# Performance work log

Measured on AMD Instinct MI355X. Metric: run time of the kernel, lower is better.

## Reference

```python
import jax, jax.numpy as jnp
import numpy as np

INPUT, HIDDEN, OUTPUT = 256, 512, 256
BATCH, SEQ = 64, 2048


def setup_inputs() -> dict:
    key = jax.random.key(0)
    ks = jax.random.split(key, 5)
    x = jax.random.normal(ks[0], (BATCH, SEQ, INPUT), dtype=jnp.float32)
    W_x = jax.random.normal(ks[1], (INPUT, 4 * HIDDEN), dtype=jnp.float32) * 0.1
    W_h = jax.random.normal(ks[2], (HIDDEN, 4 * HIDDEN), dtype=jnp.float32) * 0.1
    b = jnp.zeros((4 * HIDDEN,), dtype=jnp.float32)
    # fc: nn.Linear(hidden, output) -> weight [OUTPUT, HIDDEN], bias [OUTPUT]
    lim = 1.0 / np.sqrt(HIDDEN)
    fc_w = jax.random.uniform(ks[3], (OUTPUT, HIDDEN), dtype=jnp.float32, minval=-lim, maxval=lim)
    fc_b = jax.random.uniform(ks[4], (OUTPUT,), dtype=jnp.float32, minval=-lim, maxval=lim)
    return {"x": x, "W_x": W_x, "W_h": W_h, "b": b, "fc_w": fc_w, "fc_b": fc_b}


def reference(x, W_x, W_h, b, fc_w, fc_b):
    B, T, _ = x.shape
    H = W_h.shape[0]
    # precompute input projections for all timesteps: [B,T,4H]
    xg = jnp.einsum('bti,ig->btg', x, W_x) + b

    def step(carry, xg_t):
        h, c = carry
        gates = xg_t + h @ W_h  # [B,4H]
        i_t, f_t, g_t, o_t = jnp.split(gates, 4, axis=-1)
        i_t = jax.nn.sigmoid(i_t)
        f_t = jax.nn.sigmoid(f_t)
        g_t = jnp.tanh(g_t)
        o_t = jax.nn.sigmoid(o_t)
        c_new = f_t * c + i_t * g_t
        h_new = o_t * jnp.tanh(c_new)
        return (h_new, c_new), None

    h0 = jnp.zeros((B, H), dtype=x.dtype)
    c0 = jnp.zeros((B, H), dtype=x.dtype)
    (h_t, c_t), _ = jax.lax.scan(step, (h0, c0), jnp.swapaxes(xg, 0, 1))
    y = h_t @ fc_w.T + fc_b
    return y, (h_t, c_t)
```

## Files before the change

### kernel.cpp

```cpp
#include <hip/hip_runtime.h>

#define B_ 64
#define T_ 2048
#define I_ 256
#define H_ 512
#define O_ 256
#define GBC 2
#define GHC 32
#define MB (B_/GBC)
#define HS (H_/GHC)
#define NC (4*HS)
#define KK (I_+H_)
#define GSTR 68

#define XSTR 528
#define XBUFB (MB*XSTR)
#define HSTR 1040
#define HOFF (2*XBUFB)
#define GOFF (HOFF + MB*HSTR)
#define LDSB (GOFF + MB*GSTR*4)

typedef __attribute__((ext_vector_type(8))) short short8;
typedef __attribute__((ext_vector_type(4))) float f32x4;
typedef __attribute__((ext_vector_type(4))) float float4v;
typedef __attribute__((ext_vector_type(4))) int int4v;

__device__ __forceinline__ unsigned short f2bf(float f) {
  union { float f; unsigned u; } v; v.f = f;
  unsigned r = v.u + 0x7fffu + ((v.u >> 16) & 1u);
  return (unsigned short)(r >> 16);
}
__device__ __forceinline__ unsigned asu(float f) { union { float f; unsigned u; } v; v.f = f; return v.u; }
__device__ __forceinline__ float asf(unsigned u) { union { unsigned u; float f; } v; v.u = u; return v.f; }

__device__ __forceinline__ short8 pack8(float4v a, float4v b) {
  short8 o;
  o[0] = (short)f2bf(a[0]); o[1] = (short)f2bf(a[1]);
  o[2] = (short)f2bf(a[2]); o[3] = (short)f2bf(a[3]);
  o[4] = (short)f2bf(b[0]); o[5] = (short)f2bf(b[1]);
  o[6] = (short)f2bf(b[2]); o[7] = (short)f2bf(b[3]);
  return o;
}

__device__ __forceinline__ void ld_x4_sc1(int4v& v, const unsigned* p) {
  asm volatile("global_load_dwordx4 %0, %1, off sc1" : "=v"(v) : "v"(p) : "memory");
}

__global__ void init_kernel(unsigned int* __restrict__ p, int n4) {
  int i = blockIdx.x * 256 + threadIdx.x;
  if (i < n4) p[i] = 0u;
}

__global__ void prep_kernel(const float* __restrict__ Wx, const float* __restrict__ Wh,
                            const float* __restrict__ bias,
                            unsigned short* __restrict__ Wcat, float* __restrict__ bcat) {
  int idx = blockIdx.x * 256 + threadIdx.x;
  int k = idx >> 11;
  int gcol = idx & 2047;
  float v = (k < I_) ? Wx[k * 2048 + gcol] : Wh[(k - I_) * 2048 + gcol];
  int gate = gcol >> 9, j = gcol & 511;
  int gh = j >> 4, jj = j & 15;
  int c = (gate << 4) | jj;
  Wcat[((size_t)(gh * NC + c) * KK) + k] = f2bf(v);
  if (k == 0) bcat[gh * NC + c] = bias[gcol];
}

__global__ __launch_bounds__(512, 1) void lstm_kernel(
    const float* __restrict__ x,
    const unsigned short* __restrict__ Wcat,
    const float* __restrict__ bcat,
    unsigned* hexf,
    float* __restrict__ hout, float* __restrict__ cout)
{
  __shared__ __align__(16) char L[LDSB];
  float* gates = reinterpret_cast<float*>(&L[GOFF]);

  const int tid = threadIdx.x;
  const int wg = blockIdx.x;
  const int gb = (wg >> 2) & 1;
  const int gh = ((wg >> 3) << 2) | (wg & 3);
  const int bbase = gb * MB;
  const int hbase = gh * HS;
  const int lane = tid & 63, wid = tid >> 6;
  const int mt = wid >> 2, nt = wid & 3;

  short8 wfrag[24];
  {
    const int col = nt * 16 + (lane & 15);
    const short8* wsrc = reinterpret_cast<const short8*>(
        Wcat + (size_t)(gh * NC + col) * KK + ((lane >> 4) * 8));
#pragma unroll
    for (int kk = 0; kk < 24; ++kk) wfrag[kk] = wsrc[kk * 4];
#pragma unroll
    for (int kk = 0; kk < 24; ++kk) asm volatile("" : "+a"(wfrag[kk]));
  }
  const float bias_l = bcat[gh * NC + nt * 16 + (lane & 15)];

  const int l31 = lane & 31, lhi = lane >> 5;
  const int crow = tid >> 4, cjj = tid & 15;
  const int arow = mt * 16 + (lane & 15);
  const int afr = (lane >> 4) * 16;

  float creg = 0.f;
  float4v xr[4];
  int bud = 1 << 20;

#pragma unroll
  for (int p = 0; p < 2; ++p) {
    const int xrow = 4 * wid + 2 * p + lhi;
    const float* xp = x + ((size_t)(bbase + xrow) * T_ + 0) * I_ + 8 * l31;
    float4v a = *reinterpret_cast<const float4v*>(xp);
    float4v b = *reinterpret_cast<const float4v*>(xp + 4);
    *reinterpret_cast<short8*>(&L[XBUFB + xrow * XSTR + 16 * l31]) = pack8(a, b);
  }
#pragma unroll
  for (int p = 0; p < 2; ++p) {
    const int xrow = 4 * wid + 2 * p + lhi;
    const float* xp = x + ((size_t)(bbase + xrow) * T_ + 1) * I_ + 8 * l31;
    xr[2 * p] = *reinterpret_cast<const float4v*>(xp);
    xr[2 * p + 1] = *reinterpret_cast<const float4v*>(xp + 4);
  }

  for (int s = 1; s <= T_; ++s) {
    const int bprev = (s - 1) & 1, bcur = s & 1;
    const unsigned tagexp = (unsigned)((s - 1) & 3);

    if (s < T_) {
#pragma unroll
      for (int p = 0; p < 2; ++p) {
        const int xrow = 4 * wid + 2 * p + lhi;
        *reinterpret_cast<short8*>(&L[((s + 1) & 1) * XBUFB + xrow * XSTR + 16 * l31]) =
            pack8(xr[2 * p], xr[2 * p + 1]);
      }
      if (s + 1 < T_) {
#pragma unroll
        for (int p = 0; p < 2; ++p) {
          const int xrow = 4 * wid + 2 * p + lhi;
          const float* xp = x + ((size_t)(bbase + xrow) * T_ + (s + 1)) * I_ + 8 * l31;
          xr[2 * p] = *reinterpret_cast<const float4v*>(xp);
          xr[2 * p + 1] = *reinterpret_cast<const float4v*>(xp + 4);
        }
      }
    }

    f32x4 acc = {bias_l, bias_l, bias_l, bias_l};
    {
      const char* xb = &L[(s & 1) * XBUFB + arow * XSTR + afr];
#pragma unroll
      for (int kk = 0; kk < 8; ++kk) {
        short8 a = *reinterpret_cast<const short8*>(xb + kk * 64);
        acc = __builtin_amdgcn_mfma_f32_16x16x32_bf16(a, wfrag[kk], acc, 0, 0, 0);
      }
    }

    int4v hv[8];
    {
      const unsigned* hb = hexf + (size_t)bprev * B_ * H_ + (size_t)bbase * H_ + 8 * lane;
      while (true) {
#pragma unroll
        for (int p = 0; p < 4; ++p) {
          const unsigned* rp = hb + (size_t)(p * 8 + wid) * H_;
          ld_x4_sc1(hv[2 * p], rp);
          ld_x4_sc1(hv[2 * p + 1], rp + 4);
        }
        asm volatile("s_waitcnt vmcnt(0)" ::: "memory");
        __builtin_amdgcn_sched_barrier(0);
        int ok = 1;
#pragma unroll
        for (int i = 0; i < 8; ++i)
#pragma unroll
          for (int j = 0; j < 4; ++j)
            ok &= (int)(((unsigned)hv[i][j] & 3u) == tagexp);
        if (__all(ok) || --bud < 0) break;
      }
    }

#pragma unroll
    for (int p = 0; p < 4; ++p) {
      float4v a, b;
#pragma unroll
      for (int j = 0; j < 4; ++j) { a[j] = asf((unsigned)hv[2 * p][j]); b[j] = asf((unsigned)hv[2 * p + 1][j]); }
      *reinterpret_cast<short8*>(&L[HOFF + (p * 8 + wid) * HSTR + 16 * lane]) = pack8(a, b);
    }
    __syncthreads();

    {
      const char* hbq = &L[HOFF + arow * HSTR + afr];
#pragma unroll
      for (int kk = 0; kk < 16; ++kk) {
        short8 a = *reinterpret_cast<const short8*>(hbq + kk * 64);
        acc = __builtin_amdgcn_mfma_f32_16x16x32_bf16(a, wfrag[8 + kk], acc, 0, 0, 0);
      }
      const int col = nt * 16 + (lane & 15);
      const int r0 = mt * 16 + ((lane >> 4) << 2);
      gates[(r0 + 0) * GSTR + col] = acc[0];
      gates[(r0 + 1) * GSTR + col] = acc[1];
      gates[(r0 + 2) * GSTR + col] = acc[2];
      gates[(r0 + 3) * GSTR + col] = acc[3];
    }
    __syncthreads();

    {
      const float* grow = &gates[crow * GSTR];
      float ig = grow[cjj], fg = grow[16 + cjj], gg = grow[32 + cjj], og = grow[48 + cjj];
      float i_ = 1.f / (1.f + __expf(-ig));
      float f_ = 1.f / (1.f + __expf(-fg));
      float g_ = 1.f - 2.f / (__expf(2.f * gg) + 1.f);
      float o_ = 1.f / (1.f + __expf(-og));
      creg = f_ * creg + i_ * g_;
      float hvf = o_ * (1.f - 2.f / (__expf(2.f * creg) + 1.f));
      unsigned tagged = (asu(hvf) & ~3u) | (unsigned)(s & 3);
      __hip_atomic_store(
          hexf + (size_t)bcur * B_ * H_ + (size_t)(bbase + crow) * H_ + hbase + cjj,
          tagged, __ATOMIC_RELAXED, __HIP_MEMORY_SCOPE_AGENT);
      if (s == T_) {
        hout[(bbase + crow) * H_ + hbase + cjj] = hvf;
        cout[(bbase + crow) * H_ + hbase + cjj] = creg;
      }
    }
  }
}

__global__ void fc_kernel(const float* __restrict__ hT, const float* __restrict__ fcw,
                          const float* __restrict__ fcb, float* __restrict__ y) {
  __shared__ float hr[H_];
  const int b = blockIdx.x, o = threadIdx.x;
  hr[o] = hT[b * H_ + o];
  hr[o + 256] = hT[b * H_ + 256 + o];
  __syncthreads();
  const float4v* w = reinterpret_cast<const float4v*>(fcw + (size_t)o * H_);
  const float4v* h4 = reinterpret_cast<const float4v*>(hr);
  float s0 = 0.f, s1 = 0.f, s2 = 0.f, s3 = 0.f;
#pragma unroll 8
  for (int k = 0; k < H_ / 4; ++k) {
    float4v wv = w[k], hv = h4[k];
    s0 += wv[0] * hv[0]; s1 += wv[1] * hv[1];
    s2 += wv[2] * hv[2]; s3 += wv[3] * hv[3];
  }
  y[b * O_ + o] = s0 + s1 + s2 + s3 + fcb[o];
}

extern "C" void kernel_launch(void* const* d_in, const int* in_sizes, int n_in,
                              void* d_out, int out_size, void* d_ws, size_t ws_size,
                              hipStream_t stream) {
  const float* x    = (const float*)d_in[0];
  const float* Wx   = (const float*)d_in[1];
  const float* Wh   = (const float*)d_in[2];
  const float* bias = (const float*)d_in[3];
  const float* fcw  = (const float*)d_in[4];
  const float* fcb  = (const float*)d_in[5];
  float* out = (float*)d_out;

  char* ws = (char*)d_ws;
  unsigned short* Wcat = (unsigned short*)ws;
  float* bcat          = (float*)(ws + 3145728);
  unsigned* hexf       = (unsigned*)(ws + 3145728 + 8192);

  init_kernel<<<dim3(256), dim3(256), 0, stream>>>((unsigned int*)hexf, 65536);
  prep_kernel<<<dim3((KK * 2048) / 256), dim3(256), 0, stream>>>(Wx, Wh, bias, Wcat, bcat);
  lstm_kernel<<<dim3(GBC * GHC), dim3(512), 0, stream>>>(
      x, Wcat, bcat, hexf, out + 16384, out + 16384 + 32768);
  fc_kernel<<<dim3(B_), dim3(256), 0, stream>>>(out + 16384, fcw, fcb, out);
}
```

Baseline: 6.240 ms.

## Issue h polling loads early and overlap with x prefetch and x-part MFMA

Moves the first round of tagged h-state loads to the top of each timestep so they are in flight while the next x tile is packed, the following x tile is prefetched and the input-projection MFMAs run. Precise vmcnt waits split the h loads from the x prefetch, and retries back off with s_sleep. Also swaps the manual bf16 rounding for packed hardware bf16 conversion intrinsics. The early first poll is more likely to see stale tags and need a retry, and the hand-counted vmcnt values must match the actual load order.

```diff
diff --git a/kernel.cpp b/kernel.cpp
--- a/kernel.cpp
+++ b/kernel.cpp
@@ -1,4 +1,5 @@
 #include <hip/hip_runtime.h>
+#include <hip/hip_bf16.h>
 
 #define B_ 64
 #define T_ 2048
@@ -31,19 +32,23 @@
   return (unsigned short)(r >> 16);
 }
 __device__ __forceinline__ unsigned asu(float f) { union { float f; unsigned u; } v; v.f = f; return v.u; }
-__device__ __forceinline__ float asf(unsigned u) { union { unsigned u; float f; } v; v.u = u; return v.f; }
-
-__device__ __forceinline__ short8 pack8(float4v a, float4v b) {
-  short8 o;
-  o[0] = (short)f2bf(a[0]); o[1] = (short)f2bf(a[1]);
-  o[2] = (short)f2bf(a[2]); o[3] = (short)f2bf(a[3]);
-  o[4] = (short)f2bf(b[0]); o[5] = (short)f2bf(b[1]);
-  o[6] = (short)f2bf(b[2]); o[7] = (short)f2bf(b[3]);
-  return o;
+
+__device__ __forceinline__ unsigned pk2(float lo, float hi) {
+  __hip_bfloat162 t = __float22bfloat162_rn(make_float2(lo, hi));
+  union { __hip_bfloat162 b; unsigned u; } v; v.b = t; return v.u;
+}
+__device__ __forceinline__ short8 pack8v(float4v a, float4v b) {
+  union { unsigned u[4]; short8 s; } r;
+  r.u[0] = pk2(a[0], a[1]); r.u[1] = pk2(a[2], a[3]);
+  r.u[2] = pk2(b[0], b[1]); r.u[3] = pk2(b[2], b[3]);
+  return r.s;
 }
 
 __device__ __forceinline__ void ld_x4_sc1(int4v& v, const unsigned* p) {
   asm volatile("global_load_dwordx4 %0, %1, off sc1" : "=v"(v) : "v"(p) : "memory");
+}
+__device__ __forceinline__ void ld_x4f(float4v& v, const float* p) {
+  asm volatile("global_load_dwordx4 %0, %1, off" : "=v"(v) : "v"(p) : "memory");
 }
 
 __global__ void init_kernel(unsigned int* __restrict__ p, int n4) {
@@ -94,11 +99,12 @@
 #pragma unroll
     for (int kk = 0; kk < 24; ++kk) asm volatile("" : "+a"(wfrag[kk]));
   }
-  const float bias_l = bcat[gh * NC + nt * 16 + (lane & 15)];
+  const int c15 = lane & 15;
+  const float bias_l = bcat[gh * NC + nt * 16 + c15];
 
   const int l31 = lane & 31, lhi = lane >> 5;
   const int crow = tid >> 4, cjj = tid & 15;
-  const int arow = mt * 16 + (lane & 15);
+  const int arow = mt * 16 + c15;
   const int afr = (lane >> 4) * 16;
 
   float creg = 0.f;
@@ -111,35 +117,45 @@
     const float* xp = x + ((size_t)(bbase + xrow) * T_ + 0) * I_ + 8 * l31;
     float4v a = *reinterpret_cast<const float4v*>(xp);
     float4v b = *reinterpret_cast<const float4v*>(xp + 4);
-    *reinterpret_cast<short8*>(&L[XBUFB + xrow * XSTR + 16 * l31]) = pack8(a, b);
+    *reinterpret_cast<short8*>(&L[XBUFB + xrow * XSTR + 16 * l31]) = pack8v(a, b);
   }
 #pragma unroll
   for (int p = 0; p < 2; ++p) {
     const int xrow = 4 * wid + 2 * p + lhi;
     const float* xp = x + ((size_t)(bbase + xrow) * T_ + 1) * I_ + 8 * l31;
-    xr[2 * p] = *reinterpret_cast<const float4v*>(xp);
-    xr[2 * p + 1] = *reinterpret_cast<const float4v*>(xp + 4);
+    ld_x4f(xr[2 * p], xp);
+    ld_x4f(xr[2 * p + 1], xp + 4);
   }
 
   for (int s = 1; s <= T_; ++s) {
     const int bprev = (s - 1) & 1, bcur = s & 1;
     const unsigned tagexp = (unsigned)((s - 1) & 3);
 
+    int4v hv[8];
+    const unsigned* hb = hexf + (size_t)bprev * B_ * H_ + (size_t)bbase * H_ + 8 * lane;
+#pragma unroll
+    for (int i = 0; i < 8; ++i)
+      ld_x4_sc1(hv[i], hb + (size_t)(8 * (i >> 1) + wid) * H_ + 4 * (i & 1));
+
+    asm volatile("s_waitcnt vmcnt(8)" ::: "memory");
+    __builtin_amdgcn_sched_barrier(0);
+
     if (s < T_) {
 #pragma unroll
       for (int p = 0; p < 2; ++p) {
         const int xrow = 4 * wid + 2 * p + lhi;
         *reinterpret_cast<short8*>(&L[((s + 1) & 1) * XBUFB + xrow * XSTR + 16 * l31]) =
-            pack8(xr[2 * p], xr[2 * p + 1]);
-      }
-      if (s + 1 < T_) {
-#pragma unroll
-        for (int p = 0; p < 2; ++p) {
-          const int xrow = 4 * wid + 2 * p + lhi;
-          const float* xp = x + ((size_t)(bbase + xrow) * T_ + (s + 1)) * I_ + 8 * l31;
-          xr[2 * p] = *reinterpret_cast<const float4v*>(xp);
-          xr[2 * p + 1] = *reinterpret_cast<const float4v*>(xp + 4);
-        }
+            pack8v(xr[2 * p], xr[2 * p + 1]);
+      }
+    }
+
+    if (s + 1 < T_) {
+#pragma unroll
+      for (int p = 0; p < 2; ++p) {
+        const int xrow = 4 * wid + 2 * p + lhi;
+        const float* xp = x + ((size_t)(bbase + xrow) * T_ + (s + 1)) * I_ + 8 * l31;
+        ld_x4f(xr[2 * p], xp);
+        ld_x4f(xr[2 * p + 1], xp + 4);
       }
     }
 
@@ -153,34 +169,31 @@
       }
     }
 
-    int4v hv[8];
-    {
-      const unsigned* hb = hexf + (size_t)bprev * B_ * H_ + (size_t)bbase * H_ + 8 * lane;
-      while (true) {
-#pragma unroll
-        for (int p = 0; p < 4; ++p) {
-          const unsigned* rp = hb + (size_t)(p * 8 + wid) * H_;
-          ld_x4_sc1(hv[2 * p], rp);
-          ld_x4_sc1(hv[2 * p + 1], rp + 4);
-        }
-        asm volatile("s_waitcnt vmcnt(0)" ::: "memory");
-        __builtin_amdgcn_sched_barrier(0);
-        int ok = 1;
-#pragma unroll
-        for (int i = 0; i < 8; ++i)
-#pragma unroll
-          for (int j = 0; j < 4; ++j)
-            ok &= (int)(((unsigned)hv[i][j] & 3u) == tagexp);
-        if (__all(ok) || --bud < 0) break;
-      }
+    if (s + 1 < T_) { asm volatile("s_waitcnt vmcnt(4)" ::: "memory"); }
+    else            { asm volatile("s_waitcnt vmcnt(0)" ::: "memory"); }
+    __builtin_amdgcn_sched_barrier(0);
+    while (true) {
+      int ok = 1;
+#pragma unroll
+      for (int i = 0; i < 8; ++i)
+#pragma unroll
+        for (int j = 0; j < 4; ++j)
+          ok &= (int)(((unsigned)hv[i][j] & 3u) == tagexp);
+      if (__all(ok) || --bud < 0) break;
+      __builtin_amdgcn_s_sleep(1);
+#pragma unroll
+      for (int i = 0; i < 8; ++i)
+        ld_x4_sc1(hv[i], hb + (size_t)(8 * (i >> 1) + wid) * H_ + 4 * (i & 1));
+      asm volatile("s_waitcnt vmcnt(0)" ::: "memory");
+      __builtin_amdgcn_sched_barrier(0);
     }
 
 #pragma unroll
     for (int p = 0; p < 4; ++p) {
-      float4v a, b;
-#pragma unroll
-      for (int j = 0; j < 4; ++j) { a[j] = asf((unsigned)hv[2 * p][j]); b[j] = asf((unsigned)hv[2 * p + 1][j]); }
-      *reinterpret_cast<short8*>(&L[HOFF + (p * 8 + wid) * HSTR + 16 * lane]) = pack8(a, b);
+      union { int4v i; float4v f; } u0, u1;
+      u0.i = hv[2 * p]; u1.i = hv[2 * p + 1];
+      *reinterpret_cast<short8*>(&L[HOFF + (8 * p + wid) * HSTR + 16 * lane]) =
+          pack8v(u0.f, u1.f);
     }
     __syncthreads();
 
@@ -191,7 +204,7 @@
         short8 a = *reinterpret_cast<const short8*>(hbq + kk * 64);
         acc = __builtin_amdgcn_mfma_f32_16x16x32_bf16(a, wfrag[8 + kk], acc, 0, 0, 0);
       }
-      const int col = nt * 16 + (lane & 15);
+      const int col = nt * 16 + c15;
       const int r0 = mt * 16 + ((lane >> 4) << 2);
       gates[(r0 + 0) * GSTR + col] = acc[0];
       gates[(r0 + 1) * GSTR + col] = acc[1];
@@ -209,10 +222,10 @@
       float o_ = 1.f / (1.f + __expf(-og));
       creg = f_ * creg + i_ * g_;
       float hvf = o_ * (1.f - 2.f / (__expf(2.f * creg) + 1.f));
-      unsigned tagged = (asu(hvf) & ~3u) | (unsigned)(s & 3);
       __hip_atomic_store(
           hexf + (size_t)bcur * B_ * H_ + (size_t)(bbase + crow) * H_ + hbase + cjj,
-          tagged, __ATOMIC_RELAXED, __HIP_MEMORY_SCOPE_AGENT);
+          (asu(hvf) & ~3u) | (unsigned)(s & 3),
+          __ATOMIC_RELAXED, __HIP_MEMORY_SCOPE_AGENT);
       if (s == T_) {
         hout[(bbase + crow) * H_ + hbase + cjj] = hvf;
         cout[(bbase + crow) * H_ + hbase + cjj] = creg;
```

New measurement: 9.757 ms. +56.4%, slower.
